# Optimization experiments

Hardware: AMD Instinct MI355X
Metric: run time of the kernel (lower is better)

The kernel has to match this reference:

```python
import jax, jax.numpy as jnp
import numpy as np

BETA_F = 1000.0
BETA_B = 1.0
CLAMP = 12.0
B, C, H, W = 4, 1, 1024, 1024
N_NODES = 262144  # nodes per max-tree


def soft_mask(logits):
    # forward sigmoid with beta_f gain and +-12 clamp (clamp_logits=True)
    return jax.nn.sigmoid(jnp.clip(BETA_F * logits, -CLAMP, CLAMP))


def tree_filter(sigma, levels, parent):
    """Differentiable connected filtering on one max-tree.
    Node value = level(root) + sum over root->node path of sigma_j*(level_j - level_parent_j),
    computed with pointer-doubling ancestor sums (log N gather passes).
    sigma, levels: (N,), parent: (N,) int32 with parent[0]==0 (root).
    """
    N = sigma.shape[0]
    delta = levels - levels[parent]          # per-node gray-level increment
    c = (sigma * delta).at[0].set(levels[0])  # root contributes its level
    # sentinel node N with contribution 0 and self-pointer, terminates chains
    acc = jnp.concatenate([c, jnp.zeros((1,), c.dtype)])
    ptr = jnp.concatenate([parent.at[0].set(N), jnp.full((1,), N, parent.dtype)])
    steps = int(np.ceil(np.log2(N))) + 1
    for _ in range(steps):
        acc, ptr = acc + acc[ptr], ptr[ptr]
    return acc[:N]


def setup_inputs() -> dict:
    rng = np.random.default_rng(0)
    T = B * C  # one tree per (b, c) image
    idx = np.arange(N_NODES)
    # topologically ordered random tree: parent[i] in [0, i), parent[0] = 0
    parent = np.floor(rng.random((T, N_NODES)) * idx).astype(np.int32)
    # monotone increasing gray levels: ancestor-sum of positive increments
    inc = (rng.random((T, N_NODES)) + 0.1).astype(np.float32)
    acc = np.concatenate([inc, np.zeros((T, 1), np.float32)], 1)
    ptr = np.concatenate([parent, np.full((T, 1), N_NODES, np.int64)], 1)
    ptr[:, 0] = N_NODES
    for _ in range(int(np.ceil(np.log2(N_NODES))) + 1):
        acc = acc + np.take_along_axis(acc, ptr, 1)
        ptr = np.take_along_axis(ptr, ptr, 1)
    levels = acc[:, :N_NODES]
    attr_norm = rng.random((T, N_NODES)).astype(np.float32)  # minmax01-normalized attribute
    pixel_to_node = rng.integers(0, N_NODES, (T, H * W)).astype(np.int32)
    x = rng.standard_normal((B, C, H, W)).astype(np.float32)
    return {
        "x": jnp.asarray(x),
        "attr_norm": jnp.asarray(attr_norm),
        "levels": jnp.asarray(levels),
        "thr": jnp.full((1,), 0.5, jnp.float32),  # torch init.constant_(p, 0.5)
        "parent": jnp.asarray(parent),
        "pixel_to_node": jnp.asarray(pixel_to_node),
    }


def reference(x, attr_norm, levels, thr, parent, pixel_to_node):
    # logits = attr_scaled - threshold_norm, per node, per tree
    sigma = soft_mask(attr_norm - thr.reshape(()))          # (T, N)
    v = jax.vmap(tree_filter)(sigma, levels, parent)         # (T, N) filtered node values
    y = jnp.take_along_axis(v, pixel_to_node, axis=1)        # node -> pixel gather
    return y.reshape(B, C, H, W)  # top_hat=False, num_groups=1 -> out_channels=C
```

## Files before the change

kernel.cpp:

```cpp
#include <hip/hip_runtime.h>

#define NT 4
#define NN 262144
#define NMASK (NN - 1)
#define HW 1048576

__global__ __launch_bounds__(256) void k_build(const float* __restrict__ attr,
                                               const float* __restrict__ levels,
                                               const float* __restrict__ thr,
                                               const int* __restrict__ parent,
                                               int2* __restrict__ cmb) {
    int i = blockIdx.x * 256 + threadIdx.x;
    int n = i & NMASK;
    int tbase = i ^ n;
    int p = parent[i] & NMASK;
    float lv = levels[i];
    float lp = levels[tbase | p];
    float z = 1000.0f * (attr[i] - thr[0]);
    z = fminf(fmaxf(z, -12.0f), 12.0f);
    float s = 1.0f / (1.0f + __expf(-z));
    float c = s * (lv - lp);
    if (n == 0) { c = lv; p = 0; }
    int2 o;
    o.x = p;
    o.y = __float_as_int(c);
    cmb[i] = o;
}

__global__ __launch_bounds__(256) void k_walk(const int2* __restrict__ cmb,
                                              float* __restrict__ v) {
    int b = blockIdx.x * 1024;
    int tbase = b & ~NMASK;
    const int2* ctree = cmb + tbase;

    int   cur[4];
    float acc[4];
#pragma unroll
    for (int k = 0; k < 4; ++k) {
        cur[k] = (b - tbase) + threadIdx.x + k * 256;
        acc[k] = 0.0f;
    }

    int alive = 0xF;
    for (int it = 0; it < 64 && alive; ++it) {
#pragma unroll
        for (int k = 0; k < 4; ++k) {
            int c_ = cur[k];
            int2 pc = ctree[c_];
            float w = (alive >> k) & 1 ? 1.0f : 0.0f;
            acc[k] += w * __int_as_float(pc.y);
            if (c_ == 0) alive &= ~(1 << k);
            cur[k] = (c_ == 0) ? 0 : (pc.x & NMASK);
        }
    }

#pragma unroll
    for (int k = 0; k < 4; ++k)
        v[b + threadIdx.x + k * 256] = acc[k];
}

__global__ __launch_bounds__(256) void k_pix(const float* __restrict__ v,
                                             const int* __restrict__ p2n,
                                             float* __restrict__ y) {
    int i = blockIdx.x * 256 + threadIdx.x;
    int4 idx = ((const int4*)p2n)[i];
    int pix0 = i << 2;
    int t = pix0 >> 20;
    const float* vt = v + (t << 18);
    float4 o;
    o.x = vt[idx.x & NMASK];
    o.y = vt[idx.y & NMASK];
    o.z = vt[idx.z & NMASK];
    o.w = vt[idx.w & NMASK];
    ((float4*)y)[i] = o;
}

extern "C" void kernel_launch(void* const* d_in, const int* in_sizes, int n_in,
                              void* d_out, int out_size, void* d_ws, size_t ws_size,
                              hipStream_t stream) {
    const float* attr   = (const float*)d_in[1];
    const float* levels = (const float*)d_in[2];
    const float* thr    = (const float*)d_in[3];
    const int*   parent = (const int*)d_in[4];
    const int*   p2n    = (const int*)d_in[5];
    float*       y      = (float*)d_out;

    int2*  cmb = (int2*)d_ws;
    float* v   = (float*)((char*)d_ws + (size_t)NT * NN * sizeof(int2));

    k_build<<<NT * NN / 256, 256, 0, stream>>>(attr, levels, thr, parent, cmb);
    k_walk <<<NT * NN / 1024, 256, 0, stream>>>(cmb, v);
    k_pix  <<<NT * HW / 4 / 256, 256, 0, stream>>>(v, p2n, y);
}
```

Measured before the change: 147.2 us.

## Precompute prefix node values and stop ancestor walks at the prefix

Adds a kernel that fully resolves filtered values for the first KPRE nodes of each tree. The main walk then stops as soon as a chain reaches a node below KPRE and adds its precomputed value. Because parents are topologically ordered with random indices, this should shorten chains near the root. Walks also exit early using a wave-wide any, and blocks are swizzled so consecutive blocks interleave across trees. The cost is an extra kernel launch and a serial dependency between the prefix and walk stages.

```diff
diff --git a/kernel.cpp b/kernel.cpp
--- a/kernel.cpp
+++ b/kernel.cpp
@@ -4,69 +4,93 @@
 #define NN 262144
 #define NMASK (NN - 1)
 #define HW 1048576
+#define KPRE 16384
+
+#define SWIZ(b, tree, chunk)                \
+    int tree  = ((b) & 7) >> 1;             \
+    int chunk = (((b) >> 3) << 1) | ((b) & 1);
 
 __global__ __launch_bounds__(256) void k_build(const float* __restrict__ attr,
                                                const float* __restrict__ levels,
                                                const float* __restrict__ thr,
                                                const int* __restrict__ parent,
                                                int2* __restrict__ cmb) {
-    int i = blockIdx.x * 256 + threadIdx.x;
-    int n = i & NMASK;
-    int tbase = i ^ n;
+    SWIZ(blockIdx.x, tree, chunk)
+    int n = chunk * 256 + threadIdx.x;
+    int i = (tree << 18) + n;
     int p = parent[i] & NMASK;
     float lv = levels[i];
-    float lp = levels[tbase | p];
+    float lp = levels[(tree << 18) | p];
     float z = 1000.0f * (attr[i] - thr[0]);
     z = fminf(fmaxf(z, -12.0f), 12.0f);
     float s = 1.0f / (1.0f + __expf(-z));
     float c = s * (lv - lp);
     if (n == 0) { c = lv; p = 0; }
-    int2 o;
-    o.x = p;
-    o.y = __float_as_int(c);
-    cmb[i] = o;
+    cmb[i] = make_int2(p, __float_as_int(c));
+}
+
+__global__ __launch_bounds__(256) void k_prefix(const int2* __restrict__ cmb,
+                                                float* __restrict__ v) {
+    SWIZ(blockIdx.x, tree, chunk)
+    int node = chunk * 256 + threadIdx.x;
+    const int2* ctree = cmb + (tree << 18);
+    float acc = 0.0f;
+    int cur = node;
+    bool alive = true;
+    for (int it = 0; it < 64 && __any(alive); ++it) {
+        if (alive) {
+            int2 rec = ctree[cur];
+            acc += __int_as_float(rec.y);
+            if (cur == 0) alive = false;
+            else cur = rec.x;
+        }
+    }
+    v[(tree << 18) + node] = acc;
 }
 
 __global__ __launch_bounds__(256) void k_walk(const int2* __restrict__ cmb,
                                               float* __restrict__ v) {
-    int b = blockIdx.x * 1024;
-    int tbase = b & ~NMASK;
-    const int2* ctree = cmb + tbase;
+    SWIZ(blockIdx.x, tree, chunk)
+    int base = KPRE + chunk * 1024;
+    const int2*  ctree = cmb + (tree << 18);
+    const float* vtree = v + (tree << 18);
 
     int   cur[4];
     float acc[4];
+    int alive = 0xF;
 #pragma unroll
     for (int k = 0; k < 4; ++k) {
-        cur[k] = (b - tbase) + threadIdx.x + k * 256;
+        cur[k] = base + threadIdx.x + k * 256;
         acc[k] = 0.0f;
     }
-
-    int alive = 0xF;
-    for (int it = 0; it < 64 && alive; ++it) {
+    for (int it = 0; it < 64 && __any(alive); ++it) {
 #pragma unroll
         for (int k = 0; k < 4; ++k) {
-            int c_ = cur[k];
-            int2 pc = ctree[c_];
-            float w = (alive >> k) & 1 ? 1.0f : 0.0f;
-            acc[k] += w * __int_as_float(pc.y);
-            if (c_ == 0) alive &= ~(1 << k);
-            cur[k] = (c_ == 0) ? 0 : (pc.x & NMASK);
+            if (alive & (1 << k)) {
+                int2 rec = ctree[cur[k]];
+                acc[k] += __int_as_float(rec.y);
+                int nxt = rec.x;
+                if (nxt < KPRE) {
+                    acc[k] += vtree[nxt];
+                    alive &= ~(1 << k);
+                } else {
+                    cur[k] = nxt;
+                }
+            }
         }
     }
-
 #pragma unroll
     for (int k = 0; k < 4; ++k)
-        v[b + threadIdx.x + k * 256] = acc[k];
+        v[(tree << 18) + base + threadIdx.x + k * 256] = acc[k];
 }
 
 __global__ __launch_bounds__(256) void k_pix(const float* __restrict__ v,
                                              const int* __restrict__ p2n,
                                              float* __restrict__ y) {
-    int i = blockIdx.x * 256 + threadIdx.x;
+    SWIZ(blockIdx.x, tree, chunk)
+    int i = (tree << 18) + chunk * 256 + threadIdx.x;
     int4 idx = ((const int4*)p2n)[i];
-    int pix0 = i << 2;
-    int t = pix0 >> 20;
-    const float* vt = v + (t << 18);
+    const float* vt = v + (tree << 18);
     float4 o;
     o.x = vt[idx.x & NMASK];
     o.y = vt[idx.y & NMASK];
@@ -88,7 +112,8 @@
     int2*  cmb = (int2*)d_ws;
     float* v   = (float*)((char*)d_ws + (size_t)NT * NN * sizeof(int2));
 
-    k_build<<<NT * NN / 256, 256, 0, stream>>>(attr, levels, thr, parent, cmb);
-    k_walk <<<NT * NN / 1024, 256, 0, stream>>>(cmb, v);
-    k_pix  <<<NT * HW / 4 / 256, 256, 0, stream>>>(v, p2n, y);
+    k_build <<<NT * NN / 256, 256, 0, stream>>>(attr, levels, thr, parent, cmb);
+    k_prefix<<<NT * KPRE / 256, 256, 0, stream>>>(cmb, v);
+    k_walk  <<<NT * (NN - KPRE) / 1024, 256, 0, stream>>>(cmb, v);
+    k_pix   <<<NT * HW / 4 / 256, 256, 0, stream>>>(v, p2n, y);
 }
```

Result: faster. 135.5 us (-7.9%).
